# Optimization experiments

Measured on AMD Instinct MI355X. Metric: run time of the kernel, lower is better.

Reference implementation:

```python
import jax, jax.numpy as jnp
import numpy as np

N_HEADS = 16
N_EMBED = 1024
HEAD = N_EMBED // N_HEADS
NEG = -1e10


def setup_inputs() -> dict:
    key = jax.random.key(0)
    ks = jax.random.split(key, 12)
    B, Tq, Tk, C = 4, 2048, 2048, N_EMBED
    s = 1.0 / np.sqrt(C)
    return {
        "x": jax.random.normal(ks[0], (B, Tq, C), jnp.float32),
        "features": jax.random.normal(ks[1], (B, Tk, C), jnp.float32),
        "mask": jax.random.randint(ks[2], (B, 1, 1, Tk), 0, 2, jnp.int32),
        "wq": jax.random.normal(ks[3], (C, C), jnp.float32) * s,
        "bq": jnp.zeros((C,), jnp.float32),
        "wk": jax.random.normal(ks[4], (C, C), jnp.float32) * s,
        "bk": jnp.zeros((C,), jnp.float32),
        "wv": jax.random.normal(ks[5], (C, C), jnp.float32) * s,
        "bv": jnp.zeros((C,), jnp.float32),
        "wo": jax.random.normal(ks[6], (C, C), jnp.float32) * s,
        "bo": jnp.zeros((C,), jnp.float32),
    }


def reference(x, features, mask, wq, bq, wk, bk, wv, bv, wo, bo):
    B, Tq, C = x.shape
    Tk = features.shape[1]
    # project and split heads: [B, H, T, Dh]
    q = (x @ wq + bq).reshape(B, Tq, N_HEADS, HEAD).transpose(0, 2, 1, 3)
    k = (features @ wk + bk).reshape(B, Tk, N_HEADS, HEAD).transpose(0, 2, 1, 3)
    v = (features @ wv + bv).reshape(B, Tk, N_HEADS, HEAD).transpose(0, 2, 1, 3)
    attn = jnp.einsum("bhqd,bhkd->bhqk", q, k) / np.sqrt(HEAD)
    attn = jnp.where(mask == 0, NEG, attn)
    attn = jax.nn.softmax(attn, axis=-1)  # dropout p=0 (eval)
    out = jnp.einsum("bhqk,bhkd->bhqd", attn, v)
    out = out.transpose(0, 2, 1, 3).reshape(B, Tq, C)
    return out @ wo + bo
```

## Files before the change

### kernel.cpp

```cpp
#include <hip/hip_runtime.h>
#include <stdint.h>
#include <type_traits>

typedef __attribute__((ext_vector_type(8))) short bf16x8;
typedef __attribute__((ext_vector_type(4))) float f32x4;
typedef __attribute__((ext_vector_type(16))) float f32x16;

#define BB 4
#define NH 16
#define TT 2048
#define HD 64
#define CC 1024

__device__ __forceinline__ unsigned short f2bf(float f) {
  unsigned int u = __builtin_bit_cast(unsigned int, f);
  u += 0x7fff + ((u >> 16) & 1);
  return (unsigned short)(u >> 16);
}

__device__ __forceinline__ float fast_exp2(float x) {
#if __has_builtin(__builtin_amdgcn_exp2f)
  return __builtin_amdgcn_exp2f(x);
#else
  return exp2f(x);
#endif
}

__device__ __forceinline__ unsigned int cvtpk(float lo, float hi) {
  unsigned int r;
  asm("v_cvt_pk_bf16_f32 %0, %1, %2" : "=v"(r) : "v"(lo), "v"(hi));
  return r;
}

__device__ __forceinline__ void plswap(unsigned int& a, unsigned int& b) {
#if __has_builtin(__builtin_amdgcn_permlane32_swap)
  auto r = __builtin_amdgcn_permlane32_swap(a, b, false, false);
  a = r[0];
  b = r[1];
#else
  unsigned int as = __shfl_xor((int)a, 32), bs = __shfl_xor((int)b, 32);
  bool hi = (threadIdx.x & 32) != 0;
  unsigned int na = hi ? bs : a;
  unsigned int nb = hi ? b : as;
  a = na; b = nb;
#endif
}

__device__ __forceinline__ float partner32(float x, bool hi) {
  unsigned int a = __builtin_bit_cast(unsigned int, x), b = a;
  plswap(a, b);
  return __builtin_bit_cast(float, hi ? a : b);
}

__device__ __forceinline__ void g2l16(const void* g, void* s) {
  __builtin_amdgcn_global_load_lds(
      (const __attribute__((address_space(1))) unsigned int*)g,
      (__attribute__((address_space(3))) unsigned int*)s, 16, 0, 0);
}

__global__ __launch_bounds__(256) void cast2(
    const float* __restrict__ x, const float* __restrict__ ft,
    unsigned short* __restrict__ xb, unsigned short* __restrict__ fb, int n) {
  const float* in = blockIdx.y ? ft : x;
  unsigned short* out = blockIdx.y ? fb : xb;
  int i = (blockIdx.x * 256 + threadIdx.x) * 4;
  if (i >= n) return;
  float4 v = *(const float4*)(in + i);
  ushort4 o;
  o.x = f2bf(v.x); o.y = f2bf(v.y); o.z = f2bf(v.z); o.w = f2bf(v.w);
  *(ushort4*)(out + i) = o;
}

__global__ __launch_bounds__(256) void make_m01(
    const int* __restrict__ mask, float* __restrict__ m01, int n) {
  int i = blockIdx.x * 256 + threadIdx.x;
  if (i < n) m01[i] = mask[i] ? 1.0f : 0.0f;
}

__global__ __launch_bounds__(256) void transpose_cast_w4(
    const float* __restrict__ wq, const float* __restrict__ wk,
    const float* __restrict__ wv, const float* __restrict__ wo,
    unsigned short* __restrict__ wqkvt, unsigned short* __restrict__ wot) {
  __shared__ float tile[32][33];
  const int z = blockIdx.z;
  const float* w = (z == 0) ? wq : (z == 1) ? wk : (z == 2) ? wv : wo;
  unsigned short* wt = (z < 3) ? wqkvt + (size_t)z * CC * CC : wot;
  int nb = blockIdx.x * 32, kb = blockIdx.y * 32;
  int tx = threadIdx.x, ty = threadIdx.y;
#pragma unroll
  for (int r = ty; r < 32; r += 8)
    tile[r][tx] = w[(size_t)(kb + r) * CC + nb + tx];
  __syncthreads();
#pragma unroll
  for (int r = ty; r < 32; r += 8)
    wt[(size_t)(nb + r) * CC + kb + tx] = f2bf(tile[tx][r]);
}

__global__ __launch_bounds__(256) void gemm_qkv(
    const unsigned short* __restrict__ xb, const unsigned short* __restrict__ fb,
    const unsigned short* __restrict__ Wt,
    const float* __restrict__ bq, const float* __restrict__ bk,
    const float* __restrict__ bv, const float* __restrict__ m01,
    unsigned short* __restrict__ Qb, unsigned short* __restrict__ Kb,
    unsigned short* __restrict__ Vtb, float qscale) {
  __shared__ unsigned short As[128 * 32];
  __shared__ unsigned short Bs[128 * 32];
  int lin = blockIdx.y * gridDim.x + blockIdx.x;
  int cpx = (gridDim.x * gridDim.y) >> 3;
  int sw = (lin & 7) * cpx + (lin >> 3);
  const int n0g = (sw % 24) * 128;
  const int m0 = (sw / 24) * 128;
  const int sec = n0g >> 10;
  const int n0 = n0g & (CC - 1);
  const unsigned short* A = (sec == 0) ? xb : fb;
  const unsigned short* Bt = Wt + (size_t)n0g * CC;

  const int t = threadIdx.x, l = t & 63, w = t >> 6;
  const int lr = l & 15, lg = l >> 4;
  const int wr = w >> 1, wc = w & 1;
  f32x4 acc[4][4] = {};
  for (int k0 = 0; k0 < CC; k0 += 32) {
#pragma unroll
    for (int i = 0; i < 2; ++i) {
      int c = w * 64 + l + i * 256;
      int row = c >> 2, cb = (c & 3) * 8;
      g2l16(A + (size_t)(m0 + row) * CC + k0 + cb, (char*)As + c * 16);
      g2l16(Bt + (size_t)row * CC + k0 + cb, (char*)Bs + c * 16);
    }
    __syncthreads();
    bf16x8 af[4], bfr[4];
#pragma unroll
    for (int mi = 0; mi < 4; ++mi)
      af[mi] = *(const bf16x8*)(As + (wr * 64 + mi * 16 + lr) * 32 + lg * 8);
#pragma unroll
    for (int nj = 0; nj < 4; ++nj)
      bfr[nj] = *(const bf16x8*)(Bs + (wc * 64 + nj * 16 + lr) * 32 + lg * 8);
#pragma unroll
    for (int mi = 0; mi < 4; ++mi)
#pragma unroll
      for (int nj = 0; nj < 4; ++nj)
        acc[mi][nj] = __builtin_amdgcn_mfma_f32_16x16x32_bf16(
            af[mi], bfr[nj], acc[mi][nj], 0, 0, 0);
    __syncthreads();
  }
  const float* bp = (sec == 0) ? bq : (sec == 1) ? bk : bv;
  const float scale = (sec == 0) ? qscale : 1.0f;
#pragma unroll
  for (int mi = 0; mi < 4; ++mi) {
#pragma unroll
    for (int nj = 0; nj < 4; ++nj) {
      int col = n0 + wc * 64 + nj * 16 + lr;
      float bias = bp[col];
#pragma unroll
      for (int j = 0; j < 4; ++j) {
        int rowm = m0 + wr * 64 + mi * 16 + lg * 4 + j;
        float v = (acc[mi][nj][j] + bias) * scale;
        int b_ = rowm >> 11, tq = rowm & (TT - 1);
        int h_ = col >> 6, d_ = col & (HD - 1);
        if (sec < 2) {
          unsigned short* dst = (sec == 0) ? Qb : Kb;
          dst[((size_t)((b_ * NH + h_) * TT + tq) << 6) + d_] = f2bf(v);
        } else {
          v *= m01[rowm];
          Vtb[((size_t)((b_ * NH + h_) * HD + d_) * TT) + tq] = f2bf(v);
        }
      }
    }
  }
}

__global__ __launch_bounds__(256) void gemm_out(
    const unsigned short* __restrict__ A, const unsigned short* __restrict__ Bt,
    const float* __restrict__ bias, float* __restrict__ Out) {
  __shared__ unsigned short As[128 * 32];
  __shared__ unsigned short Bs[128 * 32];
  int lin = blockIdx.y * gridDim.x + blockIdx.x;
  int cpx = (gridDim.x * gridDim.y) >> 3;
  int sw = (lin & 7) * cpx + (lin >> 3);
  const int n0 = (sw % 8) * 128;
  const int m0 = (sw / 8) * 128;
  const int t = threadIdx.x, l = t & 63, w = t >> 6;
  const int lr = l & 15, lg = l >> 4;
  const int wr = w >> 1, wc = w & 1;
  f32x4 acc[4][4] = {};
  for (int k0 = 0; k0 < CC; k0 += 32) {
#pragma unroll
    for (int i = 0; i < 2; ++i) {
      int c = w * 64 + l + i * 256;
      int row = c >> 2, cb = (c & 3) * 8;
      g2l16(A + (size_t)(m0 + row) * CC + k0 + cb, (char*)As + c * 16);
      g2l16(Bt + (size_t)(n0 + row) * CC + k0 + cb, (char*)Bs + c * 16);
    }
    __syncthreads();
    bf16x8 af[4], bfr[4];
#pragma unroll
    for (int mi = 0; mi < 4; ++mi)
      af[mi] = *(const bf16x8*)(As + (wr * 64 + mi * 16 + lr) * 32 + lg * 8);
#pragma unroll
    for (int nj = 0; nj < 4; ++nj)
      bfr[nj] = *(const bf16x8*)(Bs + (wc * 64 + nj * 16 + lr) * 32 + lg * 8);
#pragma unroll
    for (int mi = 0; mi < 4; ++mi)
#pragma unroll
      for (int nj = 0; nj < 4; ++nj)
        acc[mi][nj] = __builtin_amdgcn_mfma_f32_16x16x32_bf16(
            af[mi], bfr[nj], acc[mi][nj], 0, 0, 0);
    __syncthreads();
  }
#pragma unroll
  for (int mi = 0; mi < 4; ++mi) {
#pragma unroll
    for (int nj = 0; nj < 4; ++nj) {
      int col = n0 + wc * 64 + nj * 16 + lr;
      float bv = bias[col];
#pragma unroll
      for (int j = 0; j < 4; ++j) {
        int rowm = m0 + wr * 64 + mi * 16 + lg * 4 + j;
        Out[(size_t)rowm * CC + col] = acc[mi][nj][j] + bv;
      }
    }
  }
}

__global__ __launch_bounds__(256) void attn_fwd8(
    const unsigned short* __restrict__ Q, const unsigned short* __restrict__ K,
    const unsigned short* __restrict__ Vt, const float* __restrict__ m01,
    unsigned short* __restrict__ O) {
  __shared__ __attribute__((aligned(64))) char ldsb[40960];
  const int t = threadIdx.x, l = t & 63, w = t >> 6;
  const int q5 = l & 31, hig = l >> 5;
  const bool hib = hig != 0;
  int lin = blockIdx.y * gridDim.x + blockIdx.x;
  int sw = (lin & 7) * 128 + (lin >> 3);
  const int bx = sw & 15, bh = sw >> 4;
  const int b_ = bh >> 4, h_ = bh & (NH - 1);
  const int q = bx * 128 + w * 32 + q5;
  const size_t base = (size_t)bh * TT * HD;
  const unsigned short* Kg = K + base;
  const unsigned short* Vg = Vt + (size_t)bh * HD * TT;

  bf16x8 qf[4];
  {
    const unsigned short* qp = Q + base + (size_t)q * HD + 8 * hig;
#pragma unroll
    for (int dk = 0; dk < 4; ++dk) qf[dk] = *(const bf16x8*)(qp + dk * 16);
  }

  int ka[4];
  {
    int swz = (q5 & 7) << 4;
#pragma unroll
    for (int dk = 0; dk < 4; ++dk)
      ka[dk] = q5 * 128 + ((dk * 32 + hig * 16) ^ swz);
  }
  int moff = 32768 + hig * 16;

  const int s1 = t + 256;
  const int r0 = t >> 3, c0 = (t & 7) * 16, x0 = c0 ^ ((r0 & 7) << 4);
  const int r1 = s1 >> 3, c1 = (s1 & 7) * 16, x1 = c1 ^ ((r1 & 7) << 4);
  const unsigned short* gk0 = Kg + r0 * HD + (x0 >> 1);
  const unsigned short* gk1 = Kg + r1 * HD + (x1 >> 1);
  const unsigned short* gv0 = Vg + (size_t)r0 * TT + (x0 >> 1);
  const unsigned short* gv1 = Vg + (size_t)r1 * TT + (x1 >> 1);

  auto stage = [&](int boff) {
    g2l16(gk0, ldsb + t * 16 + boff);
    g2l16(gk1, ldsb + t * 16 + 4096 + boff);
    g2l16(gv0, ldsb + 16384 + t * 16 + boff);
    g2l16(gv1, ldsb + 16384 + t * 16 + 4096 + boff);
    gk0 += 4096; gk1 += 4096; gv0 += 64; gv1 += 64;
  };

  f32x16 ot[2];
#pragma unroll
  for (int i = 0; i < 16; ++i) { ot[0][i] = 0.f; ot[1][i] = 0.f; }
  float l0 = 0.f, l1 = 0.f, l2 = 0.f, l3 = 0.f;

  {
    const float* mg = m01 + (size_t)b_ * TT;
#pragma unroll
    for (int i = 0; i < 2; ++i) {
      int s = t + i * 256;
      g2l16(mg + s * 4, ldsb + 32768 + s * 16);
    }
  }
  stage(0);
  asm volatile("s_waitcnt vmcnt(0)" ::: "memory");
  __syncthreads();

  auto compute = [&](auto Bc) {
    constexpr int BO = decltype(Bc)::value;
    constexpr int MO = BO ? 256 : 0;
    f32x16 s[2] = {};
    __builtin_amdgcn_s_setprio(1);
#pragma unroll
    for (int dk = 0; dk < 4; ++dk) {
      bf16x8 kf0 = *(const bf16x8*)(ldsb + ka[dk] + BO);
      bf16x8 kf1 = *(const bf16x8*)(ldsb + ka[dk] + 4096 + BO);
      s[0] = __builtin_amdgcn_mfma_f32_32x32x16_bf16(kf0, qf[dk], s[0], 0, 0, 0);
      s[1] = __builtin_amdgcn_mfma_f32_32x32x16_bf16(kf1, qf[dk], s[1], 0, 0, 0);
    }
    __builtin_amdgcn_s_setprio(0);

    unsigned int wl[2][4], wh[2][4];
#pragma unroll
    for (int kk = 0; kk < 2; ++kk)
#pragma unroll
      for (int g = 0; g < 4; ++g) {
        int i = g * 4;
        float e0 = fast_exp2(s[kk][i + 0]);
        float e1 = fast_exp2(s[kk][i + 1]);
        float e2 = fast_exp2(s[kk][i + 2]);
        float e3 = fast_exp2(s[kk][i + 3]);
        f32x4 mk = *(const f32x4*)(ldsb + moff + MO + kk * 128 + g * 32);
        l0 = fmaf(e0, mk[0], l0);
        l1 = fmaf(e1, mk[1], l1);
        l2 = fmaf(e2, mk[2], l2);
        l3 = fmaf(e3, mk[3], l3);
        wl[kk][g] = cvtpk(e0, e1);
        wh[kk][g] = cvtpk(e2, e3);
      }

    bf16x8 pa[4];
#pragma unroll
    for (int ks = 0; ks < 4; ++ks) {
      const int kk = ks >> 1, gA = 2 * (ks & 1), gB = gA + 1;
      unsigned int a0 = wl[kk][gA], b0 = wl[kk][gB];
      unsigned int a1 = wh[kk][gA], b1 = wh[kk][gB];
      plswap(a0, b0);
      plswap(a1, b1);
      unsigned int pw[4] = {a0, a1, b0, b1};
      pa[ks] = *(bf16x8*)pw;
    }

    __builtin_amdgcn_s_setprio(1);
#pragma unroll
    for (int ks = 0; ks < 4; ++ks) {
      bf16x8 vf0 = *(const bf16x8*)(ldsb + ka[ks] + 16384 + BO);
      bf16x8 vf1 = *(const bf16x8*)(ldsb + ka[ks] + 16384 + 4096 + BO);
      ot[0] = __builtin_amdgcn_mfma_f32_32x32x16_bf16(vf0, pa[ks], ot[0], 0, 0, 0);
      ot[1] = __builtin_amdgcn_mfma_f32_32x32x16_bf16(vf1, pa[ks], ot[1], 0, 0, 0);
    }
    __builtin_amdgcn_s_setprio(0);
  };

  for (int j = 0; j < 16; ++j) {
    stage(8192);
    compute(std::integral_constant<int, 0>{});
    asm volatile("s_waitcnt vmcnt(0)" ::: "memory");
    __syncthreads();
    if (j < 15) stage(0);
    compute(std::integral_constant<int, 8192>{});
    asm volatile("s_waitcnt vmcnt(0)" ::: "memory");
    __syncthreads();
    moff += 512;
  }

  float l_ = (l0 + l1) + (l2 + l3);
  float l_tot = l_ + partner32(l_, hib);
  const float inv = 1.f / l_tot;
  unsigned short* orow = O + ((size_t)(b_ * TT) + q) * CC + h_ * 64 + 4 * hig;
#pragma unroll
  for (int dt = 0; dt < 2; ++dt)
#pragma unroll
    for (int g = 0; g < 4; ++g) {
      unsigned short pk4[4];
#pragma unroll
      for (int j = 0; j < 4; ++j) pk4[j] = f2bf(ot[dt][4 * g + j] * inv);
      *(ushort4*)(orow + dt * 32 + 8 * g) = *(ushort4*)pk4;
    }
}

extern "C" void kernel_launch(void* const* d_in, const int* in_sizes, int n_in,
                              void* d_out, int out_size, void* d_ws, size_t ws_size,
                              hipStream_t stream) {
  const float* x  = (const float*)d_in[0];
  const float* ft = (const float*)d_in[1];
  const int* mask = (const int*)d_in[2];
  const float* wq = (const float*)d_in[3];
  const float* bq = (const float*)d_in[4];
  const float* wk = (const float*)d_in[5];
  const float* bk = (const float*)d_in[6];
  const float* wv = (const float*)d_in[7];
  const float* bv = (const float*)d_in[8];
  const float* wo = (const float*)d_in[9];
  const float* bo = (const float*)d_in[10];
  float* out = (float*)d_out;

  char* ws = (char*)d_ws;
  const size_t NTOK = (size_t)BB * TT;
  const size_t SB = NTOK * CC * 2;
  unsigned short* xb   = (unsigned short*)ws; ws += SB;
  unsigned short* fb   = (unsigned short*)ws; ws += SB;
  unsigned short* Qb   = (unsigned short*)ws; ws += SB;
  unsigned short* Kb   = (unsigned short*)ws; ws += SB;
  unsigned short* Vtb  = (unsigned short*)ws; ws += SB;
  unsigned short* AO   = (unsigned short*)ws; ws += SB;
  unsigned short* wqkvt = (unsigned short*)ws; ws += (size_t)3 * CC * CC * 2;
  unsigned short* wot   = (unsigned short*)ws; ws += (size_t)CC * CC * 2;
  float* m01 = (float*)ws; ws += NTOK * 4;

  int ncast = (int)(NTOK * CC);
  dim3 gc(ncast / 4 / 256, 2);
  cast2<<<gc, 256, 0, stream>>>(x, ft, xb, fb, ncast);
  dim3 tb(32, 8), tg(32, 32, 4);
  transpose_cast_w4<<<tg, tb, 0, stream>>>(wq, wk, wv, wo, wqkvt, wot);
  make_m01<<<(int)(NTOK / 256), 256, 0, stream>>>(mask, m01, (int)NTOK);

  const float qscale = 0.125f * 1.44269504f;
  dim3 gq(24, 64);
  gemm_qkv<<<gq, 256, 0, stream>>>(xb, fb, wqkvt, bq, bk, bv, m01,
                                   Qb, Kb, Vtb, qscale);

  dim3 ga(16, 64);
  attn_fwd8<<<ga, 256, 0, stream>>>(Qb, Kb, Vtb, m01, AO);

  dim3 go(8, 64);
  gemm_out<<<go, 256, 0, stream>>>(AO, wot, bo, out);
}
```

Before: 241.5 us.

## Double-buffer LDS tiles in QKV and output projection GEMMs

Both projection GEMMs now use two LDS buffers for the A and B tiles. The next K-slice is loaded with async global-to-LDS copies while MFMAs run on the current buffer, which hides global load latency and halves the barriers per K step. Address computation is hoisted into pointers that are incremented each step, and compute offsets become compile-time constants. In exchange, LDS use per block doubles to 32 KB, which may lower occupancy.

New measurement: 268.9 us. +11.3%, slower.

```diff
diff --git a/kernel.cpp b/kernel.cpp
--- a/kernel.cpp
+++ b/kernel.cpp
@@ -103,8 +103,8 @@
     const float* __restrict__ bv, const float* __restrict__ m01,
     unsigned short* __restrict__ Qb, unsigned short* __restrict__ Kb,
     unsigned short* __restrict__ Vtb, float qscale) {
-  __shared__ unsigned short As[128 * 32];
-  __shared__ unsigned short Bs[128 * 32];
+  __shared__ unsigned short As[2][128 * 32];
+  __shared__ unsigned short Bs[2][128 * 32];
   int lin = blockIdx.y * gridDim.x + blockIdx.x;
   int cpx = (gridDim.x * gridDim.y) >> 3;
   int sw = (lin & 7) * cpx + (lin >> 3);
@@ -118,31 +118,58 @@
   const int t = threadIdx.x, l = t & 63, w = t >> 6;
   const int lr = l & 15, lg = l >> 4;
   const int wr = w >> 1, wc = w & 1;
+
+  const int ra = t >> 2, cb8 = (t & 3) * 8;
+  const unsigned short* gA0 = A + (size_t)(m0 + ra) * CC + cb8;
+  const unsigned short* gA1 = A + (size_t)(m0 + 64 + ra) * CC + cb8;
+  const unsigned short* gB0 = Bt + (size_t)ra * CC + cb8;
+  const unsigned short* gB1 = Bt + (size_t)(64 + ra) * CC + cb8;
+  auto stage = [&](int buf) {
+    char* ab = (char*)As + buf * 8192;
+    char* bb = (char*)Bs + buf * 8192;
+    g2l16(gA0, ab + t * 16);
+    g2l16(gA1, ab + t * 16 + 4096);
+    g2l16(gB0, bb + t * 16);
+    g2l16(gB1, bb + t * 16 + 4096);
+    gA0 += 32; gA1 += 32; gB0 += 32; gB1 += 32;
+  };
+
+  const int aoff = (wr * 64 + lr) * 64 + lg * 16;
+  const int boff = (wc * 64 + lr) * 64 + lg * 16;
   f32x4 acc[4][4] = {};
-  for (int k0 = 0; k0 < CC; k0 += 32) {
-#pragma unroll
-    for (int i = 0; i < 2; ++i) {
-      int c = w * 64 + l + i * 256;
-      int row = c >> 2, cb = (c & 3) * 8;
-      g2l16(A + (size_t)(m0 + row) * CC + k0 + cb, (char*)As + c * 16);
-      g2l16(Bt + (size_t)row * CC + k0 + cb, (char*)Bs + c * 16);
-    }
-    __syncthreads();
+
+  stage(0);
+  asm volatile("s_waitcnt vmcnt(0)" ::: "memory");
+  __syncthreads();
+
+  auto compute = [&](auto Bc) {
+    constexpr int BO = decltype(Bc)::value;
     bf16x8 af[4], bfr[4];
 #pragma unroll
     for (int mi = 0; mi < 4; ++mi)
-      af[mi] = *(const bf16x8*)(As + (wr * 64 + mi * 16 + lr) * 32 + lg * 8);
+      af[mi] = *(const bf16x8*)((const char*)As + BO + aoff + mi * 1024);
 #pragma unroll
     for (int nj = 0; nj < 4; ++nj)
-      bfr[nj] = *(const bf16x8*)(Bs + (wc * 64 + nj * 16 + lr) * 32 + lg * 8);
+      bfr[nj] = *(const bf16x8*)((const char*)Bs + BO + boff + nj * 1024);
 #pragma unroll
     for (int mi = 0; mi < 4; ++mi)
 #pragma unroll
       for (int nj = 0; nj < 4; ++nj)
         acc[mi][nj] = __builtin_amdgcn_mfma_f32_16x16x32_bf16(
             af[mi], bfr[nj], acc[mi][nj], 0, 0, 0);
-    __syncthreads();
-  }
+  };
+
+  for (int j = 0; j < 16; ++j) {
+    stage(1);
+    compute(std::integral_constant<int, 0>{});
+    asm volatile("s_waitcnt vmcnt(0)" ::: "memory");
+    __syncthreads();
+    if (j < 15) stage(0);
+    compute(std::integral_constant<int, 8192>{});
+    asm volatile("s_waitcnt vmcnt(0)" ::: "memory");
+    __syncthreads();
+  }
+
   const float* bp = (sec == 0) ? bq : (sec == 1) ? bk : bv;
   const float scale = (sec == 0) ? qscale : 1.0f;
 #pragma unroll
@@ -172,8 +199,8 @@
 __global__ __launch_bounds__(256) void gemm_out(
     const unsigned short* __restrict__ A, const unsigned short* __restrict__ Bt,
     const float* __restrict__ bias, float* __restrict__ Out) {
-  __shared__ unsigned short As[128 * 32];
-  __shared__ unsigned short Bs[128 * 32];
+  __shared__ unsigned short As[2][128 * 32];
+  __shared__ unsigned short Bs[2][128 * 32];
   int lin = blockIdx.y * gridDim.x + blockIdx.x;
   int cpx = (gridDim.x * gridDim.y) >> 3;
   int sw = (lin & 7) * cpx + (lin >> 3);
@@ -182,31 +209,58 @@
   const int t = threadIdx.x, l = t & 63, w = t >> 6;
   const int lr = l & 15, lg = l >> 4;
   const int wr = w >> 1, wc = w & 1;
+
+  const int ra = t >> 2, cb8 = (t & 3) * 8;
+  const unsigned short* gA0 = A + (size_t)(m0 + ra) * CC + cb8;
+  const unsigned short* gA1 = A + (size_t)(m0 + 64 + ra) * CC + cb8;
+  const unsigned short* gB0 = Bt + (size_t)(n0 + ra) * CC + cb8;
+  const unsigned short* gB1 = Bt + (size_t)(n0 + 64 + ra) * CC + cb8;
+  auto stage = [&](int buf) {
+    char* ab = (char*)As + buf * 8192;
+    char* bb = (char*)Bs + buf * 8192;
+    g2l16(gA0, ab + t * 16);
+    g2l16(gA1, ab + t * 16 + 4096);
+    g2l16(gB0, bb + t * 16);
+    g2l16(gB1, bb + t * 16 + 4096);
+    gA0 += 32; gA1 += 32; gB0 += 32; gB1 += 32;
+  };
+
+  const int aoff = (wr * 64 + lr) * 64 + lg * 16;
+  const int boff = (wc * 64 + lr) * 64 + lg * 16;
   f32x4 acc[4][4] = {};
-  for (int k0 = 0; k0 < CC; k0 += 32) {
-#pragma unroll
-    for (int i = 0; i < 2; ++i) {
-      int c = w * 64 + l + i * 256;
-      int row = c >> 2, cb = (c & 3) * 8;
-      g2l16(A + (size_t)(m0 + row) * CC + k0 + cb, (char*)As + c * 16);
-      g2l16(Bt + (size_t)(n0 + row) * CC + k0 + cb, (char*)Bs + c * 16);
-    }
-    __syncthreads();
+
+  stage(0);
+  asm volatile("s_waitcnt vmcnt(0)" ::: "memory");
+  __syncthreads();
+
+  auto compute = [&](auto Bc) {
+    constexpr int BO = decltype(Bc)::value;
     bf16x8 af[4], bfr[4];
 #pragma unroll
     for (int mi = 0; mi < 4; ++mi)
-      af[mi] = *(const bf16x8*)(As + (wr * 64 + mi * 16 + lr) * 32 + lg * 8);
+      af[mi] = *(const bf16x8*)((const char*)As + BO + aoff + mi * 1024);
 #pragma unroll
     for (int nj = 0; nj < 4; ++nj)
-      bfr[nj] = *(const bf16x8*)(Bs + (wc * 64 + nj * 16 + lr) * 32 + lg * 8);
+      bfr[nj] = *(const bf16x8*)((const char*)Bs + BO + boff + nj * 1024);
 #pragma unroll
     for (int mi = 0; mi < 4; ++mi)
 #pragma unroll
       for (int nj = 0; nj < 4; ++nj)
         acc[mi][nj] = __builtin_amdgcn_mfma_f32_16x16x32_bf16(
             af[mi], bfr[nj], acc[mi][nj], 0, 0, 0);
-    __syncthreads();
-  }
+  };
+
+  for (int j = 0; j < 16; ++j) {
+    stage(1);
+    compute(std::integral_constant<int, 0>{});
+    asm volatile("s_waitcnt vmcnt(0)" ::: "memory");
+    __syncthreads();
+    if (j < 15) stage(0);
+    compute(std::integral_constant<int, 8192>{});
+    asm volatile("s_waitcnt vmcnt(0)" ::: "memory");
+    __syncthreads();
+  }
+
 #pragma unroll
   for (int mi = 0; mi < 4; ++mi) {
 #pragma unroll
```

## Rewrite QKV GEMM as 256x256 double-buffered 8-wave kernel with swizzled LDS

Applied to the files above, without the earlier changes.

Replaces the 128x128, 4-wave QKV projection GEMM with a 256x256 tile, 512-thread kernel. It uses a 64 KB double-buffered LDS ring with XOR-swizzled layout to avoid bank conflicts, and prefetches the next K-slab while computing the current one. MFMA phases are wrapped in setprio and sched_barrier to keep the compute and load phases interleaved. The aim is more data reuse per tile and hiding global-load latency, at the cost of higher LDS and register use, which may lower occupancy.

After: 272.6 us. 1.13x slower.

```diff
diff --git a/kernel.cpp b/kernel.cpp
--- a/kernel.cpp
+++ b/kernel.cpp
@@ -96,65 +96,102 @@
     wt[(size_t)(nb + r) * CC + kb + tx] = f2bf(tile[tx][r]);
 }
 
-__global__ __launch_bounds__(256) void gemm_qkv(
+__global__ __launch_bounds__(512) void gemm_qkv8(
     const unsigned short* __restrict__ xb, const unsigned short* __restrict__ fb,
     const unsigned short* __restrict__ Wt,
     const float* __restrict__ bq, const float* __restrict__ bk,
     const float* __restrict__ bv, const float* __restrict__ m01,
     unsigned short* __restrict__ Qb, unsigned short* __restrict__ Kb,
     unsigned short* __restrict__ Vtb, float qscale) {
-  __shared__ unsigned short As[128 * 32];
-  __shared__ unsigned short Bs[128 * 32];
-  int lin = blockIdx.y * gridDim.x + blockIdx.x;
-  int cpx = (gridDim.x * gridDim.y) >> 3;
-  int sw = (lin & 7) * cpx + (lin >> 3);
-  const int n0g = (sw % 24) * 128;
-  const int m0 = (sw / 24) * 128;
-  const int sec = n0g >> 10;
-  const int n0 = n0g & (CC - 1);
-  const unsigned short* A = (sec == 0) ? xb : fb;
-  const unsigned short* Bt = Wt + (size_t)n0g * CC;
-
+  __shared__ __attribute__((aligned(128))) char lds[65536];
   const int t = threadIdx.x, l = t & 63, w = t >> 6;
   const int lr = l & 15, lg = l >> 4;
-  const int wr = w >> 1, wc = w & 1;
-  f32x4 acc[4][4] = {};
-  for (int k0 = 0; k0 < CC; k0 += 32) {
-#pragma unroll
-    for (int i = 0; i < 2; ++i) {
-      int c = w * 64 + l + i * 256;
-      int row = c >> 2, cb = (c & 3) * 8;
-      g2l16(A + (size_t)(m0 + row) * CC + k0 + cb, (char*)As + c * 16);
-      g2l16(Bt + (size_t)row * CC + k0 + cb, (char*)Bs + c * 16);
-    }
-    __syncthreads();
-    bf16x8 af[4], bfr[4];
-#pragma unroll
-    for (int mi = 0; mi < 4; ++mi)
-      af[mi] = *(const bf16x8*)(As + (wr * 64 + mi * 16 + lr) * 32 + lg * 8);
+  const int wm = w >> 2, wn = w & 3;
+  const int lin = blockIdx.x;
+  const int sw = (lin & 7) * 48 + (lin >> 3);
+  const int mt = sw & 31, nt = sw >> 5;
+  const int m0 = mt * 256, n0g = nt * 256;
+  const int sec = n0g >> 10, n0 = n0g & (CC - 1);
+  const unsigned short* A = (sec == 0) ? xb : fb;
+
+  const int sR = t >> 2;
+  const int xsw = ((t & 3) * 16) ^ ((sR & 3) << 4);
+  const unsigned short* gA = A + (size_t)(m0 + sR) * CC + (xsw >> 1);
+  const unsigned short* gB = Wt + (size_t)(n0g + sR) * CC + (xsw >> 1);
+
+  auto stage = [&](int bufb) {
+    g2l16(gA,          lds + bufb + t * 16);
+    g2l16(gA + 131072, lds + bufb + t * 16 + 8192);
+    g2l16(gB,          lds + bufb + 16384 + t * 16);
+    g2l16(gB + 131072, lds + bufb + 16384 + t * 16 + 8192);
+    gA += 32; gB += 32;
+  };
+
+  const int colx = (lg * 16) ^ ((lr & 3) << 4);
+  const int aoff = (wm * 128 + lr) * 64 + colx;
+  const int boff = 16384 + (wn * 64 + lr) * 64 + colx;
+
+  f32x4 acc[8][4] = {};
+
+  stage(0);
+  asm volatile("s_waitcnt vmcnt(0)" ::: "memory");
+  __syncthreads();
+
+  auto tile = [&](auto BufC, bool doStage) {
+    constexpr int BO = decltype(BufC)::value;
+    if (doStage) stage(BO ^ 32768);
+    bf16x8 bf[4], af[4];
 #pragma unroll
     for (int nj = 0; nj < 4; ++nj)
-      bfr[nj] = *(const bf16x8*)(Bs + (wc * 64 + nj * 16 + lr) * 32 + lg * 8);
+      bf[nj] = *(const bf16x8*)(lds + BO + boff + nj * 1024);
+#pragma unroll
+    for (int mi = 0; mi < 4; ++mi)
+      af[mi] = *(const bf16x8*)(lds + BO + aoff + mi * 1024);
+    __builtin_amdgcn_s_setprio(1);
 #pragma unroll
     for (int mi = 0; mi < 4; ++mi)
 #pragma unroll
       for (int nj = 0; nj < 4; ++nj)
         acc[mi][nj] = __builtin_amdgcn_mfma_f32_16x16x32_bf16(
-            af[mi], bfr[nj], acc[mi][nj], 0, 0, 0);
-    __syncthreads();
-  }
+            af[mi], bf[nj], acc[mi][nj], 0, 0, 0);
+    __builtin_amdgcn_s_setprio(0);
+    __builtin_amdgcn_sched_barrier(0);
+    __builtin_amdgcn_s_barrier();
+    __builtin_amdgcn_sched_barrier(0);
+#pragma unroll
+    for (int mi = 0; mi < 4; ++mi)
+      af[mi] = *(const bf16x8*)(lds + BO + aoff + (mi + 4) * 1024);
+    __builtin_amdgcn_s_setprio(1);
+#pragma unroll
+    for (int mi = 0; mi < 4; ++mi)
+#pragma unroll
+      for (int nj = 0; nj < 4; ++nj)
+        acc[mi + 4][nj] = __builtin_amdgcn_mfma_f32_16x16x32_bf16(
+            af[mi], bf[nj], acc[mi + 4][nj], 0, 0, 0);
+    __builtin_amdgcn_s_setprio(0);
+    __builtin_amdgcn_sched_barrier(0);
+    asm volatile("s_waitcnt vmcnt(0)" ::: "memory");
+    __builtin_amdgcn_s_barrier();
+    __builtin_amdgcn_sched_barrier(0);
+  };
+
+  for (int j = 0; j < 16; ++j) {
+    tile(std::integral_constant<int, 0>{}, true);
+    tile(std::integral_constant<int, 32768>{}, j < 15);
+  }
+
   const float* bp = (sec == 0) ? bq : (sec == 1) ? bk : bv;
   const float scale = (sec == 0) ? qscale : 1.0f;
 #pragma unroll
-  for (int mi = 0; mi < 4; ++mi) {
+  for (int mi = 0; mi < 8; ++mi) {
 #pragma unroll
     for (int nj = 0; nj < 4; ++nj) {
-      int col = n0 + wc * 64 + nj * 16 + lr;
+      int col = n0 + wn * 64 + nj * 16 + lr;
       float bias = bp[col];
 #pragma unroll
-      for (int j = 0; j < 4; ++j) {
-        int rowm = m0 + wr * 64 + mi * 16 + lg * 4 + j;
-        float v = (acc[mi][nj][j] + bias) * scale;
+      for (int jj = 0; jj < 4; ++jj) {
+        int rowm = m0 + wm * 128 + mi * 16 + lg * 4 + jj;
+        float v = (acc[mi][nj][jj] + bias) * scale;
         int b_ = rowm >> 11, tq = rowm & (TT - 1);
         int h_ = col >> 6, d_ = col & (HD - 1);
         if (sec < 2) {
@@ -408,9 +445,8 @@
   make_m01<<<(int)(NTOK / 256), 256, 0, stream>>>(mask, m01, (int)NTOK);
 
   const float qscale = 0.125f * 1.44269504f;
-  dim3 gq(24, 64);
-  gemm_qkv<<<gq, 256, 0, stream>>>(xb, fb, wqkvt, bq, bk, bv, m01,
-                                   Qb, Kb, Vtb, qscale);
+  gemm_qkv8<<<384, 512, 0, stream>>>(xb, fb, wqkvt, bq, bk, bv, m01,
+                                     Qb, Kb, Vtb, qscale);
 
   dim3 ga(16, 64);
   attn_fwd8<<<ga, 256, 0, stream>>>(Qb, Kb, Vtb, m01, AO);
```
